# Kernel optimization log

Measured on AMD Instinct MI355X. Metric: run time of the kernel, lower is better.

## Reference

```python
import jax, jax.numpy as jnp
import numpy as np

# I-BERT IntSoftmax constants
X0 = -0.6931            # -ln(2)
N_SHIFT = 30.0
C0 = 0.35815147
C1 = 0.96963238 / C0    # coef[1] / coef[0]
C2 = 1.0 / C0           # coef[2] / coef[0]
OUTPUT_BIT = 8
ACT_QMAX = 2.0 ** 15 - 1.0  # QuantAct(16)


def setup_inputs() -> dict:
    key = jax.random.key(0)
    x = jax.random.normal(key, (4, 12, 1024, 1024), dtype=jnp.float32)
    # per-tensor symmetric activation scale (e.g. 8-bit style): 1/127
    scaling_factor = jnp.ones((), dtype=jnp.float32) / 127.0
    return {"x": x, "scaling_factor": scaling_factor}


def reference(x, scaling_factor):
    sf = scaling_factor
    # x_int = (x / sf).to(int32): truncation toward zero; keep float for speed
    x_int = jnp.trunc(x / sf)
    x_int = x_int - jnp.max(x_int, axis=-1, keepdims=True)

    # int_exp: range reduction x = r + q * x0
    x0_int = jnp.floor(X0 / sf)                       # negative integer
    x_int = jnp.maximum(x_int, N_SHIFT * x0_int)
    q = jnp.floor(x_int / x0_int)                     # 0 <= q <= 30
    r = x_int - x0_int * q

    # int_polynomial on remainder r
    b_int = jnp.floor(C1 / sf)
    c_int = jnp.floor(C2 / (sf * sf))
    z = r * (r + b_int) + c_int
    exp_scale = C0 * sf * sf
    exp_int = jnp.maximum(jnp.floor(z * jnp.exp2(N_SHIFT - q)), 0.0)
    exp_scale = exp_scale / (2.0 ** N_SHIFT)

    # QuantAct(16): dynamic per-tensor symmetric requantization
    max_abs = jnp.maximum(jnp.abs(jnp.min(exp_int)), jnp.abs(jnp.max(exp_int)))
    max_abs = jnp.maximum(max_abs, jnp.float32(np.finfo(np.float32).eps))
    act_scale = max_abs / ACT_QMAX
    # exp_q = clamp(round(exp_int/act_scale)) * act_scale; then exp_int = exp_q/act_scale
    exp_int = jnp.clip(jnp.round(exp_int / act_scale), -ACT_QMAX, ACT_QMAX)

    # integer normalization
    exp_int_sum = jnp.sum(exp_int, axis=-1, keepdims=True)
    factor = jnp.floor((2.0 ** 32) / exp_int_sum)
    out_int = jnp.floor(exp_int * factor / (2.0 ** (32 - OUTPUT_BIT + 1)))
    out_scale = jnp.float32(2.0 / (2.0 ** OUTPUT_BIT))
    return out_int * out_scale, out_scale
```

## Files before the change

kernel.cpp:

```cpp
#include <hip/hip_runtime.h>
#include <cstdint>


typedef float floatx4 __attribute__((ext_vector_type(4)));

static __device__ __forceinline__ float wave_max(float v) {
#pragma unroll
    for (int m = 32; m >= 1; m >>= 1) v = fmaxf(v, __shfl_xor(v, m, 64));
    return v;
}
static __device__ __forceinline__ float wave_sum(float v) {
#pragma unroll
    for (int m = 32; m >= 1; m >>= 1) v += __shfl_xor(v, m, 64);
    return v;
}

static __device__ __forceinline__ float div_cr(float a, float b, float y) {
    float q0 = a * y;
    float r0 = fmaf(-b, q0, a);
    return fmaf(r0, y, q0);
}

__global__ __launch_bounds__(256) void intsoftmax_ibert_kernel(
    const float* __restrict__ x, const float* __restrict__ sfp,
    float* __restrict__ out, long long n_total)
{
    const float sfv = sfp[0];

    const float x0i = floorf(-0.6931f / sfv);
    const float bi  = floorf((float)(0.96963238 / 0.35815147) / sfv);
    const float ci  = floorf((float)(1.0 / 0.35815147) / (sfv * sfv));
    const float x0a = -x0i;
    const float hi  = 30.0f * x0a;
    const float as  = (ci * 1073741824.0f) / 32767.0f;

    const float ysf = (float)(1.0 / (double)sfv);
    const float yas = (float)(1.0 / (double)as);
    const float rpu = __uint_as_float(__float_as_uint((float)(1.0 / (double)x0a)) + 1);

    const int lane = threadIdx.x & 63;
    const int wv   = threadIdx.x >> 6;
    const long long row = (long long)blockIdx.x * 4 + wv;

    const floatx4* __restrict__ xr   = (const floatx4*)(x + row * 1024);
    floatx4* __restrict__       orow = (floatx4*)(out + row * 1024);

    float xi[16];
#pragma unroll
    for (int k = 0; k < 4; ++k) {
        floatx4 a = xr[lane + 64 * k];
#pragma unroll
        for (int j = 0; j < 4; ++j)
            xi[4 * k + j] = truncf(div_cr(a[j], sfv, ysf));
    }

    float m = xi[0];
#pragma unroll
    for (int i = 1; i < 16; ++i) m = fmaxf(m, xi[i]);
    m = wave_max(m);

    float eq[16];
    float lsum = 0.0f;
#pragma unroll
    for (int i = 0; i < 16; ++i) {
        float vp = fminf(m - xi[i], hi);
        float q  = floorf(vp * rpu);
        float r  = fmaf(x0a, q, -vp);
        float z  = fmaf(r, r + bi, ci);
        float p2 = __uint_as_float((uint32_t)(157 - (int)q) << 23);
        float e  = z * p2;
        float t  = rintf(div_cr(e, as, yas));
        t = fminf(t, 32767.0f);
        eq[i] = t;
        lsum += t;
    }
    float s = wave_sum(lsum);
    float factor = floorf(4294967296.0f / s);

#pragma unroll
    for (int k = 0; k < 4; ++k) {
        floatx4 o;
#pragma unroll
        for (int j = 0; j < 4; ++j)
            o[j] = floorf(eq[4 * k + j] * factor * (1.0f / 33554432.0f)) * 0.0078125f;
        __builtin_nontemporal_store(o, &orow[lane + 64 * k]);
    }

    if (blockIdx.x == 0 && threadIdx.x == 0) out[n_total] = 0.0078125f;
}

extern "C" void kernel_launch(void* const* d_in, const int* in_sizes, int n_in,
                              void* d_out, int out_size, void* d_ws, size_t ws_size,
                              hipStream_t stream) {
    const float* x  = (const float*)d_in[0];
    const float* sf = (const float*)d_in[1];
    float* out = (float*)d_out;

    const long long n_total = (long long)out_size - 1;
    const int rows = (int)(n_total / 1024);
    const int grid = rows / 4;

    intsoftmax_ibert_kernel<<<grid, 256, 0, stream>>>(x, sf, out, n_total);
}
```

Measured before the change: 54.94 us.

## Process four rows per wave with software-prefetched next-row loads

Each wave now handles four consecutive rows instead of one and issues the loads for the next row before computing the current one, so memory latency overlaps with compute. The grid shrinks by four. It also folds the constant scale into the normalization factor, saving one multiply per element. The cost is higher register pressure, fewer blocks to hide latency, and a small tail-balance risk for this memory-bound kernel.

After: 56.13 us. 1.02x slower.

```diff
diff --git a/kernel.cpp b/kernel.cpp
--- a/kernel.cpp
+++ b/kernel.cpp
@@ -14,12 +14,13 @@
     for (int m = 32; m >= 1; m >>= 1) v += __shfl_xor(v, m, 64);
     return v;
 }
-
 static __device__ __forceinline__ float div_cr(float a, float b, float y) {
     float q0 = a * y;
     float r0 = fmaf(-b, q0, a);
     return fmaf(r0, y, q0);
 }
+
+#define ROWS_PER_WAVE 4
 
 __global__ __launch_bounds__(256) void intsoftmax_ibert_kernel(
     const float* __restrict__ x, const float* __restrict__ sfp,
@@ -40,50 +41,68 @@
 
     const int lane = threadIdx.x & 63;
     const int wv   = threadIdx.x >> 6;
-    const long long row = (long long)blockIdx.x * 4 + wv;
+    const long long row0 = ((long long)blockIdx.x * 4 + wv) * ROWS_PER_WAVE;
 
-    const floatx4* __restrict__ xr   = (const floatx4*)(x + row * 1024);
-    floatx4* __restrict__       orow = (floatx4*)(out + row * 1024);
-
-    float xi[16];
-#pragma unroll
-    for (int k = 0; k < 4; ++k) {
-        floatx4 a = xr[lane + 64 * k];
-#pragma unroll
-        for (int j = 0; j < 4; ++j)
-            xi[4 * k + j] = truncf(div_cr(a[j], sfv, ysf));
+    floatx4 L0, L1, L2, L3;
+    {
+        const floatx4* p = (const floatx4*)(x + row0 * 1024);
+        L0 = p[lane]; L1 = p[lane + 64]; L2 = p[lane + 128]; L3 = p[lane + 192];
     }
 
-    float m = xi[0];
 #pragma unroll
-    for (int i = 1; i < 16; ++i) m = fmaxf(m, xi[i]);
-    m = wave_max(m);
+    for (int t = 0; t < ROWS_PER_WAVE; ++t) {
+        const long long row = row0 + t;
 
-    float eq[16];
-    float lsum = 0.0f;
+        floatx4 N0, N1, N2, N3;
+        if (t < ROWS_PER_WAVE - 1) {
+            const floatx4* p = (const floatx4*)(x + (row + 1) * 1024);
+            N0 = p[lane]; N1 = p[lane + 64]; N2 = p[lane + 128]; N3 = p[lane + 192];
+        }
+
+        float xi[16];
 #pragma unroll
-    for (int i = 0; i < 16; ++i) {
-        float vp = fminf(m - xi[i], hi);
-        float q  = floorf(vp * rpu);
-        float r  = fmaf(x0a, q, -vp);
-        float z  = fmaf(r, r + bi, ci);
-        float p2 = __uint_as_float((uint32_t)(157 - (int)q) << 23);
-        float e  = z * p2;
-        float t  = rintf(div_cr(e, as, yas));
-        t = fminf(t, 32767.0f);
-        eq[i] = t;
-        lsum += t;
-    }
-    float s = wave_sum(lsum);
-    float factor = floorf(4294967296.0f / s);
+        for (int j = 0; j < 4; ++j) {
+            xi[0  + j] = truncf(div_cr(L0[j], sfv, ysf));
+            xi[4  + j] = truncf(div_cr(L1[j], sfv, ysf));
+            xi[8  + j] = truncf(div_cr(L2[j], sfv, ysf));
+            xi[12 + j] = truncf(div_cr(L3[j], sfv, ysf));
+        }
 
+        float m = xi[0];
 #pragma unroll
-    for (int k = 0; k < 4; ++k) {
-        floatx4 o;
+        for (int i = 1; i < 16; ++i) m = fmaxf(m, xi[i]);
+        m = wave_max(m);
+
+        float eq[16];
+        float lsum = 0.0f;
 #pragma unroll
-        for (int j = 0; j < 4; ++j)
-            o[j] = floorf(eq[4 * k + j] * factor * (1.0f / 33554432.0f)) * 0.0078125f;
-        __builtin_nontemporal_store(o, &orow[lane + 64 * k]);
+        for (int i = 0; i < 16; ++i) {
+            float vp = fminf(m - xi[i], hi);
+            float q  = floorf(vp * rpu);
+            float r  = fmaf(x0a, q, -vp);
+            float z  = fmaf(r, r + bi, ci);
+            float p2 = __uint_as_float((uint32_t)(157 - (int)q) << 23);
+            float e  = z * p2;
+            float t2 = rintf(div_cr(e, as, yas));
+            t2 = fminf(t2, 32767.0f);
+            eq[i] = t2;
+            lsum += t2;
+        }
+        float s = wave_sum(lsum);
+        float factor  = floorf(4294967296.0f / s);
+        float factor2 = factor * (1.0f / 33554432.0f);
+
+        floatx4* orow = (floatx4*)(out + row * 1024);
+#pragma unroll
+        for (int k = 0; k < 4; ++k) {
+            floatx4 o;
+#pragma unroll
+            for (int j = 0; j < 4; ++j)
+                o[j] = floorf(eq[4 * k + j] * factor2) * 0.0078125f;
+            __builtin_nontemporal_store(o, &orow[lane + 64 * k]);
+        }
+
+        if (t < ROWS_PER_WAVE - 1) { L0 = N0; L1 = N1; L2 = N2; L3 = N3; }
     }
 
     if (blockIdx.x == 0 && threadIdx.x == 0) out[n_total] = 0.0078125f;
@@ -98,7 +117,7 @@
 
     const long long n_total = (long long)out_size - 1;
     const int rows = (int)(n_total / 1024);
-    const int grid = rows / 4;
+    const int grid = rows / (4 * ROWS_PER_WAVE);
 
     intsoftmax_ibert_kernel<<<grid, 256, 0, stream>>>(x, sf, out, n_total);
 }
```
